# Kernel tuning notes

Measured on AMD Instinct MI355X. Metric: run time of the kernel, lower is better.

The kernel has to match this reference:

```python
import jax, jax.numpy as jnp
import numpy as np

W_WORDS, T_TOKENS, N_EMBD, N_HIDDEN = 4096, 32768, 512, 2048
MASK_DENSITY = 0.004  # ~ avg word covers a handful of char positions


def setup_inputs() -> dict:
    key = jax.random.key(0)
    k1, k2, k3, k4, k5 = jax.random.split(key, 5)
    in_words = jax.random.normal(k1, (W_WORDS, N_EMBD), dtype=jnp.float32)
    x = jax.random.normal(k2, (T_TOKENS, N_EMBD), dtype=jnp.float32)
    attention_mask = jax.random.bernoulli(k3, MASK_DENSITY, (W_WORDS, T_TOKENS))
    W_fc = jax.random.normal(k4, (N_EMBD, N_HIDDEN), dtype=jnp.float32) * (1.0 / np.sqrt(N_EMBD))
    W_proj = jax.random.normal(k5, (N_HIDDEN, N_EMBD), dtype=jnp.float32) * (1.0 / np.sqrt(N_HIDDEN))
    return {"in_words": in_words, "x": x, "attention_mask": attention_mask,
            "W_fc": W_fc, "W_proj": W_proj}


def reference(in_words, x, attention_mask, W_fc, W_proj):
    # MLP with residual (dropout = identity at eval): words [W, D]
    h = jax.nn.gelu(in_words @ W_fc, approximate=False)  # [W, H], exact GELU like nn.GELU()
    words = h @ W_proj + in_words                         # [W, D]
    # Per-word masked scatter-add into x_new. The sequential python loop
    # x_new[mask_i] += words[i] is additive across i, so it equals
    # x + mask^T @ words (mask promoted to float for the contraction).
    x_new = x + jnp.einsum('wt,wd->td', attention_mask.astype(words.dtype), words)
    return words, x_new
```

## Files before the change

kernel.cpp:

```cpp
#include <hip/hip_runtime.h>
#include <hip/hip_bf16.h>
#include <math.h>

#define W_WORDS  4096
#define T_TOKENS 32768
#define N_EMBD   512
#define N_HIDDEN 2048
#define CAP      64

typedef __attribute__((ext_vector_type(8))) short bf16x8;
typedef __attribute__((ext_vector_type(4))) float f32x4;
typedef __attribute__((ext_vector_type(4))) int   i32x4;
typedef unsigned int u32;

#define GLOBAL_AS __attribute__((address_space(1)))
#define LDS_AS    __attribute__((address_space(3)))

__global__ __launch_bounds__(256) void prep_kernel(
    const float* __restrict__ in_words, __hip_bfloat16* __restrict__ words_bf,
    const float* __restrict__ W_fc,     __hip_bfloat16* __restrict__ WfcT,
    const float* __restrict__ W_proj,   __hip_bfloat16* __restrict__ WprojT,
    int* __restrict__ counts)
{
    __shared__ float tile[32][33];
    const int b = blockIdx.x;

    if (b < 1024) {
        const size_t gid = (size_t)b * 256 + threadIdx.x;
        const float4 a0 = ((const float4*)in_words)[2 * gid];
        const float4 a1 = ((const float4*)in_words)[2 * gid + 1];
        union { __hip_bfloat16 t[8]; bf16x8 v; } u;
        u.t[0] = __float2bfloat16(a0.x); u.t[1] = __float2bfloat16(a0.y);
        u.t[2] = __float2bfloat16(a0.z); u.t[3] = __float2bfloat16(a0.w);
        u.t[4] = __float2bfloat16(a1.x); u.t[5] = __float2bfloat16(a1.y);
        u.t[6] = __float2bfloat16(a1.z); u.t[7] = __float2bfloat16(a1.w);
        *(bf16x8*)(words_bf + 8 * gid) = u.v;
        return;
    }
    if (b < 3072) {
        const float* in;  __hip_bfloat16* out; int R, C, bx, by;
        if (b < 2048) { in = W_fc;   out = WfcT;   R = N_EMBD;   C = N_HIDDEN;
                        const int l = b - 1024; bx = l & 63; by = l >> 6; }
        else          { in = W_proj; out = WprojT; R = N_HIDDEN; C = N_EMBD;
                        const int l = b - 2048; bx = l & 15; by = l >> 4; }
        const int tx = threadIdx.x & 31, ty = threadIdx.x >> 5;
        const int r0 = by * 32, c0 = bx * 32;
#pragma unroll
        for (int i = 0; i < 4; ++i) {
            const int r = ty + i * 8;
            tile[r][tx] = in[(size_t)(r0 + r) * C + c0 + tx];
        }
        __syncthreads();
#pragma unroll
        for (int i = 0; i < 4; ++i) {
            const int r = ty + i * 8;
            out[(size_t)(c0 + r) * R + r0 + tx] = __float2bfloat16(tile[tx][r]);
        }
        return;
    }
    const int idx = (b - 3072) * 1024 + (int)threadIdx.x * 4;
    *(i32x4*)(counts + idx) = (i32x4){0, 0, 0, 0};
}

template <int BM, int BN, int MODE>
__global__ __launch_bounds__(256) void gemm_bf16_mfma_kernel(
    const __hip_bfloat16* __restrict__ A,
    const __hip_bfloat16* __restrict__ BT,
    const float* __restrict__ Res,
    void* __restrict__ Cout,
    __hip_bfloat16* __restrict__ Cbf,
    int M, int N, int K)
{
    constexpr int BK = 32;
    constexpr int WM = BM / 2, WN = BN / 2;
    constexpr int FM = WM / 16, FN = WN / 16;
    constexpr int NA = (BM * 64) / 4096;
    constexpr int NB = (BN * 64) / 4096;

    __shared__ __align__(16) char smem[(BM + BN) * 64];
    char* As = smem;
    char* Bs = smem + BM * 64;

    const int tid  = threadIdx.x;
    const int lane = tid & 63;
    const int wid  = tid >> 6;
    const int wm   = wid >> 1, wn = wid & 1;
    const int bm   = blockIdx.y * BM;
    const int bn   = blockIdx.x * BN;

    f32x4 acc[FM][FN] = {};

    for (int k0 = 0; k0 < K; k0 += BK) {
#pragma unroll
        for (int a = 0; a < NA; ++a) {
            const int c    = a * 4 + wid;
            const int loff = c * 1024 + lane * 16;
            const int row  = loff >> 6;
            const int kb   = loff & 63;
            const __hip_bfloat16* src = A + (size_t)(bm + row) * K + k0 + (kb >> 1);
            __builtin_amdgcn_global_load_lds(
                (const GLOBAL_AS u32*)(const void*)src,
                (LDS_AS u32*)(void*)(As + c * 1024), 16, 0, 0);
        }
#pragma unroll
        for (int bq = 0; bq < NB; ++bq) {
            const int c    = bq * 4 + wid;
            const int loff = c * 1024 + lane * 16;
            const int row  = loff >> 6;
            const int kb   = loff & 63;
            const __hip_bfloat16* src = BT + (size_t)(bn + row) * K + k0 + (kb >> 1);
            __builtin_amdgcn_global_load_lds(
                (const GLOBAL_AS u32*)(const void*)src,
                (LDS_AS u32*)(void*)(Bs + c * 1024), 16, 0, 0);
        }
        __syncthreads();

        bf16x8 af[FM], bfq[FN];
#pragma unroll
        for (int i = 0; i < FM; ++i) {
            const int row = wm * WM + i * 16 + (lane & 15);
            af[i] = *(const bf16x8*)(As + row * 64 + (lane >> 4) * 16);
        }
#pragma unroll
        for (int j = 0; j < FN; ++j) {
            const int col = wn * WN + j * 16 + (lane & 15);
            bfq[j] = *(const bf16x8*)(Bs + col * 64 + (lane >> 4) * 16);
        }
#pragma unroll
        for (int i = 0; i < FM; ++i)
#pragma unroll
            for (int j = 0; j < FN; ++j)
                acc[i][j] = __builtin_amdgcn_mfma_f32_16x16x32_bf16(
                    af[i], bfq[j], acc[i][j], 0, 0, 0);
        __syncthreads();
    }

#pragma unroll
    for (int i = 0; i < FM; ++i) {
        const int row0 = bm + wm * WM + i * 16 + (lane >> 4) * 4;
#pragma unroll
        for (int j = 0; j < FN; ++j) {
            const int col = bn + wn * WN + j * 16 + (lane & 15);
#pragma unroll
            for (int r = 0; r < 4; ++r) {
                const int row = row0 + r;
                float v = acc[i][j][r];
                if (MODE == 0) {
                    v = 0.5f * v * (1.0f + erff(v * 0.70710678118654752440f));
                    ((__hip_bfloat16*)Cout)[(size_t)row * N + col] = __float2bfloat16(v);
                } else {
                    const float vv = v + Res[(size_t)row * N + col];
                    ((float*)Cout)[(size_t)row * N + col] = vv;
                    Cbf[(size_t)row * N + col] = __float2bfloat16(vv);
                }
            }
        }
    }
}

__global__ __launch_bounds__(256) void scan_kernel(
    const int* __restrict__ mask, int* __restrict__ counts,
    unsigned short* __restrict__ lists)
{
    const size_t base = (size_t)blockIdx.x * 4096;
#pragma unroll
    for (int k = 0; k < 4; ++k) {
        const size_t e = base + (size_t)k * 1024 + (size_t)threadIdx.x * 4;
        const i32x4 v = __builtin_nontemporal_load((const i32x4*)(mask + e));
        if ((v.x | v.y | v.z | v.w) == 0) continue;
        const int w  = (int)(e >> 15);
        const int t0 = (int)(e & (T_TOKENS - 1));
        if (v.x) { const int p = atomicAdd(&counts[t0+0], 1); if (p < CAP) lists[(size_t)(t0+0)*CAP+p] = (unsigned short)w; }
        if (v.y) { const int p = atomicAdd(&counts[t0+1], 1); if (p < CAP) lists[(size_t)(t0+1)*CAP+p] = (unsigned short)w; }
        if (v.z) { const int p = atomicAdd(&counts[t0+2], 1); if (p < CAP) lists[(size_t)(t0+2)*CAP+p] = (unsigned short)w; }
        if (v.w) { const int p = atomicAdd(&counts[t0+3], 1); if (p < CAP) lists[(size_t)(t0+3)*CAP+p] = (unsigned short)w; }
    }
}

__device__ inline void acc_bf8(f32x4& a, f32x4& b, bf16x8 r)
{
    a.x += __uint_as_float(((u32)(unsigned short)r[0]) << 16);
    a.y += __uint_as_float(((u32)(unsigned short)r[1]) << 16);
    a.z += __uint_as_float(((u32)(unsigned short)r[2]) << 16);
    a.w += __uint_as_float(((u32)(unsigned short)r[3]) << 16);
    b.x += __uint_as_float(((u32)(unsigned short)r[4]) << 16);
    b.y += __uint_as_float(((u32)(unsigned short)r[5]) << 16);
    b.z += __uint_as_float(((u32)(unsigned short)r[6]) << 16);
    b.w += __uint_as_float(((u32)(unsigned short)r[7]) << 16);
}

__global__ __launch_bounds__(256) void scatter_add_kernel(
    const float* __restrict__ x, const __hip_bfloat16* __restrict__ words_bf,
    const int* __restrict__ counts, const unsigned short* __restrict__ lists,
    float* __restrict__ x_new)
{
    const int t = __builtin_amdgcn_readfirstlane(
        (int)blockIdx.x * 4 + ((int)threadIdx.x >> 6));
    const int lane = threadIdx.x & 63;
    const size_t base = (size_t)t * N_EMBD + lane * 8;

    f32x4 s0a = __builtin_nontemporal_load((const f32x4*)(x + base));
    f32x4 s0b = __builtin_nontemporal_load((const f32x4*)(x + base + 4));
    f32x4 s1a = {0.f, 0.f, 0.f, 0.f};
    f32x4 s1b = {0.f, 0.f, 0.f, 0.f};

    const int cnt = min(counts[t], CAP);
    const unsigned short* lst = &lists[(size_t)t * CAP];

    int i = 0;
    for (; i + 2 <= cnt; i += 2) {
        const bf16x8 r0 = *(const bf16x8*)(words_bf + (size_t)lst[i]     * N_EMBD + lane * 8);
        const bf16x8 r1 = *(const bf16x8*)(words_bf + (size_t)lst[i + 1] * N_EMBD + lane * 8);
        acc_bf8(s0a, s0b, r0);
        acc_bf8(s1a, s1b, r1);
    }
    if (i < cnt) {
        const bf16x8 r0 = *(const bf16x8*)(words_bf + (size_t)lst[i] * N_EMBD + lane * 8);
        acc_bf8(s0a, s0b, r0);
    }
    s0a += s1a; s0b += s1b;
    __builtin_nontemporal_store(s0a, (f32x4*)(x_new + base));
    __builtin_nontemporal_store(s0b, (f32x4*)(x_new + base + 4));
}

extern "C" void kernel_launch(void* const* d_in, const int* in_sizes, int n_in,
                              void* d_out, int out_size, void* d_ws, size_t ws_size,
                              hipStream_t stream)
{
    const float* in_words = (const float*)d_in[0];
    const float* x        = (const float*)d_in[1];
    const int*   mask     = (const int*)d_in[2];
    const float* W_fc     = (const float*)d_in[3];
    const float* W_proj   = (const float*)d_in[4];

    float* out_words = (float*)d_out;
    float* out_x     = out_words + (size_t)W_WORDS * N_EMBD;

    char* ws = (char*)d_ws;
    __hip_bfloat16* words_bf = (__hip_bfloat16*)(ws);
    __hip_bfloat16* WfcT     = (__hip_bfloat16*)(ws + (4u << 20));
    __hip_bfloat16* WprojT   = (__hip_bfloat16*)(ws + (6u << 20));
    __hip_bfloat16* h_bf     = (__hip_bfloat16*)(ws + (8u << 20));
    __hip_bfloat16* wout_bf  = (__hip_bfloat16*)(ws + (24u << 20));
    int*            counts   = (int*)(ws + (28u << 20));
    unsigned short* lists    = (unsigned short*)(ws + (28u << 20) + T_TOKENS * 4);

    prep_kernel<<<3104, 256, 0, stream>>>(in_words, words_bf, W_fc, WfcT,
                                          W_proj, WprojT, counts);

    gemm_bf16_mfma_kernel<128, 128, 0>
        <<<dim3(N_HIDDEN / 128, W_WORDS / 128), 256, 0, stream>>>(
            words_bf, WfcT, nullptr, h_bf, nullptr, W_WORDS, N_HIDDEN, N_EMBD);

    gemm_bf16_mfma_kernel<64, 64, 1>
        <<<dim3(N_EMBD / 64, W_WORDS / 64), 256, 0, stream>>>(
            h_bf, WprojT, in_words, out_words, wout_bf, W_WORDS, N_EMBD, N_HIDDEN);

    scan_kernel<<<32768, 256, 0, stream>>>(mask, counts, lists);

    scatter_add_kernel<<<T_TOKENS / 4, 256, 0, stream>>>(
        x, wout_bf, counts, lists, out_x);
}
```

Measured before the change: 238.8 us.

## Co-schedule mask scan blocks with GEMM tiles across XCDs in fused kernels

Removes the standalone scan kernel and splits its work between the two GEMM launches. Blocks are assigned by XCD index: blocks on three XCDs run GEMM tiles and blocks on the other five run mask-scan chunks, so the memory-bound scan overlaps the compute-bound GEMMs. Both launches are much larger, and only three eighths of the CUs do GEMM work, so the GEMMs could stretch if the split ratio is unbalanced.

```diff
diff --git a/kernel.cpp b/kernel.cpp
--- a/kernel.cpp
+++ b/kernel.cpp
@@ -7,6 +7,7 @@
 #define N_EMBD   512
 #define N_HIDDEN 2048
 #define CAP      64
+#define SCAN_A   14745
 
 typedef __attribute__((ext_vector_type(8))) short bf16x8;
 typedef __attribute__((ext_vector_type(4))) float f32x4;
@@ -15,6 +16,26 @@
 
 #define GLOBAL_AS __attribute__((address_space(1)))
 #define LDS_AS    __attribute__((address_space(3)))
+
+__device__ inline void scan_mask_block(const int* __restrict__ mask,
+                                       int* __restrict__ counts,
+                                       unsigned short* __restrict__ lists,
+                                       int chunk)
+{
+    const size_t base = (size_t)chunk * 4096;
+#pragma unroll
+    for (int k = 0; k < 4; ++k) {
+        const size_t e = base + (size_t)k * 1024 + (size_t)threadIdx.x * 4;
+        const i32x4 v = __builtin_nontemporal_load((const i32x4*)(mask + e));
+        if ((v.x | v.y | v.z | v.w) == 0) continue;
+        const int w  = (int)(e >> 15);
+        const int t0 = (int)(e & (T_TOKENS - 1));
+        if (v.x) { const int p = atomicAdd(&counts[t0+0], 1); if (p < CAP) lists[(size_t)(t0+0)*CAP+p] = (unsigned short)w; }
+        if (v.y) { const int p = atomicAdd(&counts[t0+1], 1); if (p < CAP) lists[(size_t)(t0+1)*CAP+p] = (unsigned short)w; }
+        if (v.z) { const int p = atomicAdd(&counts[t0+2], 1); if (p < CAP) lists[(size_t)(t0+2)*CAP+p] = (unsigned short)w; }
+        if (v.w) { const int p = atomicAdd(&counts[t0+3], 1); if (p < CAP) lists[(size_t)(t0+3)*CAP+p] = (unsigned short)w; }
+    }
+}
 
 __global__ __launch_bounds__(256) void prep_kernel(
     const float* __restrict__ in_words, __hip_bfloat16* __restrict__ words_bf,
@@ -62,15 +83,29 @@
     *(i32x4*)(counts + idx) = (i32x4){0, 0, 0, 0};
 }
 
-template <int BM, int BN, int MODE>
-__global__ __launch_bounds__(256) void gemm_bf16_mfma_kernel(
+template <int BM, int BN, int MODE, int GEMM_XCDS>
+__global__ __launch_bounds__(256) void mega_kernel(
     const __hip_bfloat16* __restrict__ A,
     const __hip_bfloat16* __restrict__ BT,
     const float* __restrict__ Res,
     void* __restrict__ Cout,
     __hip_bfloat16* __restrict__ Cbf,
-    int M, int N, int K)
-{
+    int M, int N, int K, int nTiles, int gridX,
+    const int* __restrict__ mask, int* __restrict__ counts,
+    unsigned short* __restrict__ lists, int scanBase, int scanCount)
+{
+    const int bid = (int)blockIdx.x;
+    const int xcd = bid & 7;
+
+    if (xcd >= GEMM_XCDS) {
+        const int s = (bid >> 3) * (8 - GEMM_XCDS) + (xcd - GEMM_XCDS);
+        if (s < scanCount) scan_mask_block(mask, counts, lists, scanBase + s);
+        return;
+    }
+
+    const int r = (bid >> 3) * GEMM_XCDS + xcd;
+    if (r >= nTiles) return;
+
     constexpr int BK = 32;
     constexpr int WM = BM / 2, WN = BN / 2;
     constexpr int FM = WM / 16, FN = WN / 16;
@@ -85,8 +120,8 @@
     const int lane = tid & 63;
     const int wid  = tid >> 6;
     const int wm   = wid >> 1, wn = wid & 1;
-    const int bm   = blockIdx.y * BM;
-    const int bn   = blockIdx.x * BN;
+    const int bm   = (r / gridX) * BM;
+    const int bn   = (r % gridX) * BN;
 
     f32x4 acc[FM][FN] = {};
 
@@ -142,9 +177,9 @@
         for (int j = 0; j < FN; ++j) {
             const int col = bn + wn * WN + j * 16 + (lane & 15);
 #pragma unroll
-            for (int r = 0; r < 4; ++r) {
-                const int row = row0 + r;
-                float v = acc[i][j][r];
+            for (int rr = 0; rr < 4; ++rr) {
+                const int row = row0 + rr;
+                float v = acc[i][j][rr];
                 if (MODE == 0) {
                     v = 0.5f * v * (1.0f + erff(v * 0.70710678118654752440f));
                     ((__hip_bfloat16*)Cout)[(size_t)row * N + col] = __float2bfloat16(v);
@@ -158,25 +193,6 @@
     }
 }
 
-__global__ __launch_bounds__(256) void scan_kernel(
-    const int* __restrict__ mask, int* __restrict__ counts,
-    unsigned short* __restrict__ lists)
-{
-    const size_t base = (size_t)blockIdx.x * 4096;
-#pragma unroll
-    for (int k = 0; k < 4; ++k) {
-        const size_t e = base + (size_t)k * 1024 + (size_t)threadIdx.x * 4;
-        const i32x4 v = __builtin_nontemporal_load((const i32x4*)(mask + e));
-        if ((v.x | v.y | v.z | v.w) == 0) continue;
-        const int w  = (int)(e >> 15);
-        const int t0 = (int)(e & (T_TOKENS - 1));
-        if (v.x) { const int p = atomicAdd(&counts[t0+0], 1); if (p < CAP) lists[(size_t)(t0+0)*CAP+p] = (unsigned short)w; }
-        if (v.y) { const int p = atomicAdd(&counts[t0+1], 1); if (p < CAP) lists[(size_t)(t0+1)*CAP+p] = (unsigned short)w; }
-        if (v.z) { const int p = atomicAdd(&counts[t0+2], 1); if (p < CAP) lists[(size_t)(t0+2)*CAP+p] = (unsigned short)w; }
-        if (v.w) { const int p = atomicAdd(&counts[t0+3], 1); if (p < CAP) lists[(size_t)(t0+3)*CAP+p] = (unsigned short)w; }
-    }
-}
-
 __device__ inline void acc_bf8(f32x4& a, f32x4& b, bf16x8 r)
 {
     a.x += __uint_as_float(((u32)(unsigned short)r[0]) << 16);
@@ -248,15 +264,24 @@
     prep_kernel<<<3104, 256, 0, stream>>>(in_words, words_bf, W_fc, WfcT,
                                           W_proj, WprojT, counts);
 
-    gemm_bf16_mfma_kernel<128, 128, 0>
-        <<<dim3(N_HIDDEN / 128, W_WORDS / 128), 256, 0, stream>>>(
-            words_bf, WfcT, nullptr, h_bf, nullptr, W_WORDS, N_HIDDEN, N_EMBD);
-
-    gemm_bf16_mfma_kernel<64, 64, 1>
-        <<<dim3(N_EMBD / 64, W_WORDS / 64), 256, 0, stream>>>(
-            h_bf, WprojT, in_words, out_words, wout_bf, W_WORDS, N_EMBD, N_HIDDEN);
-
-    scan_kernel<<<32768, 256, 0, stream>>>(mask, counts, lists);
+    {
+        const int nTiles = (N_HIDDEN / 128) * (W_WORDS / 128);
+        const int groups = (SCAN_A + 4) / 5;
+        mega_kernel<128, 128, 0, 3><<<groups * 8, 256, 0, stream>>>(
+            words_bf, WfcT, nullptr, h_bf, nullptr,
+            W_WORDS, N_HIDDEN, N_EMBD, nTiles, N_HIDDEN / 128,
+            mask, counts, lists, 0, SCAN_A);
+    }
+
+    {
+        const int nTiles    = (N_EMBD / 64) * (W_WORDS / 64);
+        const int scanCount = 32768 - SCAN_A;
+        const int groups    = (scanCount + 4) / 5;
+        mega_kernel<64, 64, 1, 3><<<groups * 8, 256, 0, stream>>>(
+            h_bf, WprojT, in_words, out_words, wout_bf,
+            W_WORDS, N_EMBD, N_HIDDEN, nTiles, N_EMBD / 64,
+            mask, counts, lists, SCAN_A, scanCount);
+    }
 
     scatter_add_kernel<<<T_TOKENS / 4, 256, 0, stream>>>(
         x, wout_bf, counts, lists, out_x);
```

Result: slower. 312.6 us (+30.9%).
